# Kernel optimization log

Measured on AMD Instinct MI355X. Metric: run time of the kernel, lower is better.

The kernel has to match this reference:

```python
import jax, jax.numpy as jnp
import numpy as np

EPS = 1e-5
CHUNK = 512  # chunk of known points for the running-argmin 1-NN search


def nn_idx(unknown, known):
    """1-NN index of each unknown point into known. unknown (B,n,3), known (B,m,3) -> (B,n) int32."""
    B, n, _ = unknown.shape
    m = known.shape[1]
    u2 = jnp.sum(unknown * unknown, axis=-1)  # (B,n)
    # (num_chunks, B, CHUNK, 3)
    kc = known.reshape(B, m // CHUNK, CHUNK, 3).transpose(1, 0, 2, 3)

    def step(carry, kch):
        best_d, best_i, off = carry
        k2 = jnp.sum(kch * kch, axis=-1)  # (B,CHUNK)
        # squared distances for this chunk: (B,n,CHUNK)
        d = u2[:, :, None] - 2.0 * jnp.einsum('bnd,bcd->bnc', unknown, kch) + k2[:, None, :]
        dmin = jnp.min(d, axis=-1)
        imin = jnp.argmin(d, axis=-1).astype(jnp.int32) + off
        upd = dmin < best_d
        return (jnp.where(upd, dmin, best_d), jnp.where(upd, imin, best_i), off + CHUNK), None

    init = (jnp.full((B, n), jnp.inf, unknown.dtype),
            jnp.zeros((B, n), jnp.int32),
            jnp.int32(0))
    (_, best_i, _), _ = jax.lax.scan(step, init, kc)
    return best_i


def bn_relu(x, gamma, beta):
    """Training-mode BatchNorm over (B, n) per channel followed by ReLU. x: (B,C,n)."""
    mean = jnp.mean(x, axis=(0, 2), keepdims=True)
    var = jnp.mean(jnp.square(x - mean), axis=(0, 2), keepdims=True)  # biased, as torch BN
    y = (x - mean) * jax.lax.rsqrt(var + EPS)
    return jax.nn.relu(y * gamma[None, :, None] + beta[None, :, None])


def setup_inputs() -> dict:
    key = jax.random.key(0)
    ks = jax.random.split(key, 8)
    B, n, m, C1, C2 = 2, 65536, 16384, 128, 256
    mlp = [C2 + C1, 256, 128]
    return {
        'unknown': jax.random.normal(ks[0], (B, n, 3), jnp.float32),
        'known': jax.random.normal(ks[1], (B, m, 3), jnp.float32),
        'unknow_feats': jax.random.normal(ks[2], (B, C1, n), jnp.float32),
        'known_feats': jax.random.normal(ks[3], (B, C2, m), jnp.float32),
        'w1': jax.random.normal(ks[4], (mlp[1], mlp[0]), jnp.float32) * (1.0 / np.sqrt(mlp[0])),
        'gamma1': jnp.ones((mlp[1],), jnp.float32),
        'beta1': jnp.zeros((mlp[1],), jnp.float32),
        'w2': jax.random.normal(ks[5], (mlp[2], mlp[1]), jnp.float32) * (1.0 / np.sqrt(mlp[1])),
        'gamma2': jnp.ones((mlp[2],), jnp.float32),
        'beta2': jnp.zeros((mlp[2],), jnp.float32),
    }


def reference(unknown, known, unknow_feats, known_feats, w1, gamma1, beta1, w2, gamma2, beta2):
    idx = nn_idx(unknown, known)  # (B,n) int32
    # gather: (B,C2,m) indexed along m -> (B,C2,n)
    interpolated = jnp.take_along_axis(known_feats, idx[:, None, :], axis=2)
    new_features = jnp.concatenate([interpolated, unknow_feats], axis=1)  # (B,C1+C2,n)
    h = bn_relu(jnp.einsum('oc,bcn->bon', w1, new_features), gamma1, beta1)
    out = bn_relu(jnp.einsum('oc,bcn->bon', w2, h), gamma2, beta2)
    return out  # (B, mlp[-1], n)
```

## Files before the change

kernel.cpp:

```cpp
#include <hip/hip_runtime.h>

typedef unsigned short u16;
typedef unsigned int u32;
typedef __bf16 bf16x8 __attribute__((ext_vector_type(8)));
typedef _Float16 f16;
typedef _Float16 f16x8 __attribute__((ext_vector_type(8)));
typedef float f32x4 __attribute__((ext_vector_type(4)));
typedef float f32x16 __attribute__((ext_vector_type(16)));

#define B_ 2
#define N_ 65536
#define M_ 16384
#define C1_ 128
#define C2_ 256
#define K1_ 384
#define O1_ 256
#define O2_ 128
#define JT_ 512
#define CH_ 16
#define NCH_ ((JT_/2)/CH_)
#define EPS2_ 6.0e-3f
#define TFIN_ 1.25e-4f

__device__ __forceinline__ u16 f2bf(float f) {
    u32 u = __float_as_uint(f);
    u32 r = (u + 0x7FFFu + ((u >> 16) & 1u)) >> 16;
    return (u16)r;
}
__device__ __forceinline__ float bf2f(u16 h) {
    return __uint_as_float(((u32)h) << 16);
}
__device__ __forceinline__ u32 pack2(float lo, float hi) {
    return (u32)f2bf(lo) | ((u32)f2bf(hi) << 16);
}
__device__ __forceinline__ uint4 pack8(float4 a, float4 b) {
    uint4 r;
    r.x = pack2(a.x, a.y); r.y = pack2(a.z, a.w);
    r.z = pack2(b.x, b.y); r.w = pack2(b.z, b.w);
    return r;
}
__device__ __forceinline__ u16 h2u(f16 h) {
    union { f16 h; u16 u; } c; c.h = h; return c.u;
}

__device__ __forceinline__ float mul_rn(float a, float b) {
    float p = __fmul_rn(a, b);
    asm volatile("" : "+v"(p));
    return p;
}
__device__ __forceinline__ float sq3_np(float x, float y, float z) {
    return __fadd_rn(__fadd_rn(mul_rn(x, x), mul_rn(y, y)), mul_rn(z, z));
}
__device__ __forceinline__ float dot3_fma(float a0, float b0, float a1, float b1,
                                          float a2, float b2) {
    return fmaf(a2, b2, fmaf(a1, b1, mul_rn(a0, b0)));
}


__global__ __launch_bounds__(256) void k_prep_u(const float* __restrict__ unk,
                                                u16* __restrict__ Aprep) {
    int g = blockIdx.x * 256 + threadIdx.x;
    const float* up = unk + (size_t)g * 3;
    float tx = -2.f * up[0], ty = -2.f * up[1], tz = -2.f * up[2];
    f16 xh = (f16)tx; f16 xl = (f16)(tx - (float)xh);
    f16 yh = (f16)ty; f16 yl = (f16)(ty - (float)yh);
    f16 zh = (f16)tz; f16 zl = (f16)(tz - (float)zh);
    u16 lo[8] = {h2u(xh), h2u(xh), h2u(xl), h2u(yh), h2u(yh), h2u(yl), h2u(zh), h2u(zh)};
    u16 hi[8] = {h2u(zl), 0x3C00u, 0x3C00u, 0, 0, 0, 0, 0};
    u16* tb = Aprep + ((size_t)(g >> 5)) * 512;
    int r = g & 31;
    *(uint4*)(tb + r * 8) = *(uint4*)lo;
    *(uint4*)(tb + (r + 32) * 8) = *(uint4*)hi;
}

__global__ __launch_bounds__(256) void k_prep_k(const float* __restrict__ kn,
                                                u16* __restrict__ Bprep,
                                                float4* __restrict__ kco) {
    int g = blockIdx.x * 256 + threadIdx.x;
    const float* kp = kn + (size_t)g * 3;
    float x = kp[0], y = kp[1], z = kp[2];
    float qv = sq3_np(x, y, z);
    f16 xh = (f16)x; f16 xl = (f16)(x - (float)xh);
    f16 yh = (f16)y; f16 yl = (f16)(y - (float)yh);
    f16 zh = (f16)z; f16 zl = (f16)(z - (float)zh);
    f16 qh = (f16)qv; f16 ql = (f16)(qv - (float)qh);
    u16 lo[8] = {h2u(xh), h2u(xl), h2u(xh), h2u(yh), h2u(yl), h2u(yh), h2u(zh), h2u(zl)};
    u16 hi[8] = {h2u(zh), h2u(qh), h2u(ql), 0x3C00u, 0x3C00u, 0, 0, 0};
    u16* tb = Bprep + ((size_t)(g >> 5)) * 512;
    int r = g & 31;
    *(uint4*)(tb + r * 8) = *(uint4*)lo;
    *(uint4*)(tb + (r + 32) * 8) = *(uint4*)hi;
    kco[g] = make_float4(x, y, z, qv);
}

__global__ __launch_bounds__(256, 4) void k_nn(
        const u16* __restrict__ Aprep, const u16* __restrict__ Bprep,
        const float* __restrict__ unk, const float4* __restrict__ kco,
        unsigned long long* __restrict__ pc) {
    __shared__ u16 sB[2][CH_ * 512];
    __shared__ unsigned long long cand[256];
    __shared__ float thrS[256];
    const int t = threadIdx.x;
    const int half = blockIdx.y, b = blockIdx.z;
    const int lane = t & 63, w = t >> 6;
    const int rowbase = blockIdx.x * 256;
    const u16* at = Aprep + (((size_t)(b * N_ + rowbase + w * 64)) >> 5) * 512;
    f16x8 af0 = *(const f16x8*)(at + lane * 8);
    f16x8 af1 = *(const f16x8*)(at + 512 + lane * 8);
    const u16* Bsrc = Bprep + ((size_t)b * JT_ + (size_t)half * (JT_ / 2)) * 512;
    cand[t] = ~0ULL;

    uint4 vs0, vs1, vs2, vs3;
#define STAGEV(c) { const u16* sp = Bsrc + (size_t)(c) * (CH_ * 512) + t * 8;  \
    vs0 = *(const uint4*)sp;          vs1 = *(const uint4*)(sp + 2048);        \
    vs2 = *(const uint4*)(sp + 4096); vs3 = *(const uint4*)(sp + 6144); }
#define WRITEV(bi) { u16* dp = &sB[bi][t * 8];                                 \
    *(uint4*)dp = vs0;          *(uint4*)(dp + 2048) = vs1;                    \
    *(uint4*)(dp + 4096) = vs2; *(uint4*)(dp + 6144) = vs3; }

    const f32x16 zz = {0.f,0.f,0.f,0.f,0.f,0.f,0.f,0.f,0.f,0.f,0.f,0.f,0.f,0.f,0.f,0.f};

    f32x16 rm0, rm1;
#pragma unroll
    for (int r = 0; r < 16; ++r) { rm0[r] = 3.4e38f; rm1[r] = 3.4e38f; }

    STAGEV(0); WRITEV(0);
    __syncthreads();
    for (int c = 0; c < NCH_; ++c) {
        if (c + 1 < NCH_) STAGEV(c + 1);
        const u16* bb = sB[c & 1];
#pragma unroll 2
        for (int tp = 0; tp < CH_; tp += 2) {
            f16x8 bf0 = *(const f16x8*)(bb + tp * 512 + lane * 8);
            f16x8 bf1 = *(const f16x8*)(bb + tp * 512 + 512 + lane * 8);
            f32x16 a  = __builtin_amdgcn_mfma_f32_32x32x16_f16(af0, bf0, zz, 0, 0, 0);
            f32x16 ca = __builtin_amdgcn_mfma_f32_32x32x16_f16(af0, bf1, zz, 0, 0, 0);
#pragma unroll
            for (int r = 0; r < 16; ++r)
                rm0[r] = fminf(fminf(rm0[r], a[r]), ca[r]);
            a  = __builtin_amdgcn_mfma_f32_32x32x16_f16(af1, bf0, zz, 0, 0, 0);
            ca = __builtin_amdgcn_mfma_f32_32x32x16_f16(af1, bf1, zz, 0, 0, 0);
#pragma unroll
            for (int r = 0; r < 16; ++r)
                rm1[r] = fminf(fminf(rm1[r], a[r]), ca[r]);
        }
        __syncthreads();
        if (c + 1 < NCH_) WRITEV((c + 1) & 1);
        __syncthreads();
    }

    STAGEV(0);

#pragma unroll
    for (int r = 0; r < 16; ++r) {
        float v0 = rm0[r], v1 = rm1[r];
        v0 = fminf(v0, __shfl_xor(v0, 1));  v1 = fminf(v1, __shfl_xor(v1, 1));
        v0 = fminf(v0, __shfl_xor(v0, 2));  v1 = fminf(v1, __shfl_xor(v1, 2));
        v0 = fminf(v0, __shfl_xor(v0, 4));  v1 = fminf(v1, __shfl_xor(v1, 4));
        v0 = fminf(v0, __shfl_xor(v0, 8));  v1 = fminf(v1, __shfl_xor(v1, 8));
        v0 = fminf(v0, __shfl_xor(v0, 16)); v1 = fminf(v1, __shfl_xor(v1, 16));
        if ((lane & 31) == 0) {
            int rl = w * 64 + ((lane >> 5) << 2) + (r & 3) + 8 * (r >> 2);
            thrS[rl] = v0 + EPS2_;
            thrS[rl + 32] = v1 + EPS2_;
        }
    }
    __syncthreads();
    if (lane >= 32) {
        float tf0 = thrS[w * 64 + (lane & 31)] + TFIN_;
        float tf1 = thrS[w * 64 + 32 + (lane & 31)] + TFIN_;
        f16 h0 = (f16)(-tf0);
        af0[3] = h0; af0[4] = (f16)(-tf0 - (float)h0);
        f16 h1 = (f16)(-tf1);
        af1[3] = h1; af1[4] = (f16)(-tf1 - (float)h1);
    }
    WRITEV(0);
    __syncthreads();

    const float4* kcb = kco + (size_t)b * M_;
    const float* ub = unk + (size_t)b * N_ * 3;
    const int rloc0 = w * 64 + ((lane >> 5) << 2);
    const int jb0 = half * (M_ / 2);

    for (int c = 0; c < NCH_; ++c) {
        if (c + 1 < NCH_) STAGEV(c + 1);
        const u16* bb = sB[c & 1];
#pragma unroll 2
        for (int tt = 0; tt < CH_; ++tt) {
            f16x8 bf = *(const f16x8*)(bb + tt * 512 + lane * 8);
            f32x16 a0 = __builtin_amdgcn_mfma_f32_32x32x16_f16(af0, bf, zz, 0, 0, 0);
            f32x16 a1 = __builtin_amdgcn_mfma_f32_32x32x16_f16(af1, bf, zz, 0, 0, 0);
            float u0 = fminf(fminf(a0[0], a0[1]), a0[2]);
            float u1 = fminf(fminf(a0[3], a0[4]), a0[5]);
            float u2 = fminf(fminf(a0[6], a0[7]), a0[8]);
            float u3 = fminf(fminf(a0[9], a0[10]), a0[11]);
            float u4 = fminf(fminf(a0[12], a0[13]), a0[14]);
            float tm0 = fminf(fminf(fminf(u0, u1), a0[15]), fminf(fminf(u2, u3), u4));
            float w0 = fminf(fminf(a1[0], a1[1]), a1[2]);
            float w1 = fminf(fminf(a1[3], a1[4]), a1[5]);
            float w2 = fminf(fminf(a1[6], a1[7]), a1[8]);
            float w3 = fminf(fminf(a1[9], a1[10]), a1[11]);
            float w4 = fminf(fminf(a1[12], a1[13]), a1[14]);
            float tm1 = fminf(fminf(fminf(w0, w1), a1[15]), fminf(fminf(w2, w3), w4));
            unsigned long long m = __ballot(tm0 <= 0.f) | __ballot(tm1 <= 0.f);
            if (m) {
                int j = jb0 + (c * CH_ + tt) * 32 + (lane & 31);
                float4 kc = kcb[j];
#pragma unroll
                for (int r = 0; r < 16; ++r) {
                    if (a0[r] <= 0.f) {
                        int rl = rloc0 + (r & 3) + 8 * (r >> 2);
                        const float* up = ub + (size_t)(rowbase + rl) * 3;
                        float x = up[0], y = up[1], zc = up[2];
                        float uq = sq3_np(x, y, zc);
                        float dot = dot3_fma(x, kc.x, y, kc.y, zc, kc.z);
                        float d = __fadd_rn(fmaf(-2.0f, dot, uq), kc.w);
                        u32 db = __float_as_uint(d);
                        db = (db & 0x80000000u) ? ~db : (db | 0x80000000u);
                        atomicMin(&cand[rl], ((unsigned long long)db << 32) | (u32)j);
                    }
                    if (a1[r] <= 0.f) {
                        int rl = rloc0 + 32 + (r & 3) + 8 * (r >> 2);
                        const float* up = ub + (size_t)(rowbase + rl) * 3;
                        float x = up[0], y = up[1], zc = up[2];
                        float uq = sq3_np(x, y, zc);
                        float dot = dot3_fma(x, kc.x, y, kc.y, zc, kc.z);
                        float d = __fadd_rn(fmaf(-2.0f, dot, uq), kc.w);
                        u32 db = __float_as_uint(d);
                        db = (db & 0x80000000u) ? ~db : (db | 0x80000000u);
                        atomicMin(&cand[rl], ((unsigned long long)db << 32) | (u32)j);
                    }
                }
            }
        }
        __syncthreads();
        if (c + 1 < NCH_) WRITEV((c + 1) & 1);
        __syncthreads();
    }
    pc[((size_t)(half * B_ + b)) * N_ + rowbase + t] = cand[t];
#undef STAGEV
#undef WRITEV
}

__global__ __launch_bounds__(256) void k_nn_merge(
        const unsigned long long* __restrict__ pc, int* __restrict__ idx) {
    int g = blockIdx.x * 256 + threadIdx.x;
    unsigned long long a = pc[g];
    unsigned long long c = pc[(size_t)(B_ * N_) + g];
    idx[g] = (int)(u32)((c < a ? c : a) & 0xFFFFFFFFu);
}

__global__ __launch_bounds__(256) void k_tr_kf(const float* __restrict__ kf,
                                               u16* __restrict__ kfT) {
    __shared__ float lt[64][65];
    const int t = threadIdx.x, b = blockIdx.z;
    const int j0 = blockIdx.x * 64, c0 = blockIdx.y * 64;
    const int jl = t & 63, cl4 = t >> 6;
#pragma unroll
    for (int p = 0; p < 16; ++p) {
        int c = c0 + cl4 + p * 4;
        lt[cl4 + p * 4][jl] = kf[((size_t)(b * C2_ + c)) * M_ + j0 + jl];
    }
    __syncthreads();
    const int cl = t & 63, jr4 = t >> 6;
#pragma unroll
    for (int p = 0; p < 16; ++p) {
        int j = j0 + jr4 + p * 4;
        kfT[((size_t)(b * M_ + j)) * C2_ + c0 + cl] = f2bf(lt[cl][jr4 + p * 4]);
    }
}

__global__ __launch_bounds__(256) void k_tr_uf(const float* __restrict__ uf,
                                               u16* __restrict__ newF) {
    __shared__ float lt[64][65];
    const int t = threadIdx.x, b = blockIdx.z;
    const int i0 = blockIdx.x * 64, c0 = blockIdx.y * 64;
    const int il = t & 63, cl4 = t >> 6;
#pragma unroll
    for (int p = 0; p < 16; ++p) {
        int c = c0 + cl4 + p * 4;
        lt[cl4 + p * 4][il] = uf[((size_t)(b * C1_ + c)) * N_ + i0 + il];
    }
    __syncthreads();
    const int cl = t & 63, ir4 = t >> 6;
#pragma unroll
    for (int p = 0; p < 16; ++p) {
        int i = i0 + ir4 + p * 4;
        newF[((size_t)(b * N_ + i)) * K1_ + C2_ + c0 + cl] = f2bf(lt[cl][ir4 + p * 4]);
    }
}

__global__ __launch_bounds__(256) void k_gather(const u16* __restrict__ kfT,
                                                const int* __restrict__ idx,
                                                u16* __restrict__ newF) {
    const int t = threadIdx.x, b = blockIdx.y;
    const int il = t >> 5, qq = t & 31;
    const int i = blockIdx.x * 8 + il;
    const int j = idx[b * N_ + i];
    const uint4* src = (const uint4*)(kfT + ((size_t)(b * M_ + j)) * C2_) + qq;
    uint4* dst = (uint4*)(newF + ((size_t)(b * N_ + i)) * K1_) + qq;
    *dst = *src;
}

__global__ __launch_bounds__(256) void k_gemm1(const u16* __restrict__ newF,
                                               const float* __restrict__ w1,
                                               u16* __restrict__ y1) {
    __shared__ u16 As[128 * 40];
    __shared__ u16 Bs[128 * 40];
    const int t = threadIdx.x, b = blockIdx.z;
    const int i0 = blockIdx.x * 128, o0 = blockIdx.y * 128;
    const int lane = t & 63, wv = t >> 6, wr = wv >> 1, wc = wv & 1;
    const int col = lane & 15, q = lane >> 4;

    const int rA0 = t >> 2, sA0 = t & 3;
    const u16* aS0 = newF + ((size_t)(b * N_ + i0 + rA0)) * K1_ + sA0 * 8;
    const u16* aS1 = aS0 + (size_t)64 * K1_;
    const float* bS0 = w1 + (size_t)(o0 + rA0) * K1_ + sA0 * 8;
    const float* bS1 = bS0 + (size_t)64 * K1_;
    u16* aD0 = &As[rA0 * 40 + sA0 * 8];
    u16* aD1 = aD0 + 64 * 40;
    u16* bD0 = &Bs[rA0 * 40 + sA0 * 8];
    u16* bD1 = bD0 + 64 * 40;

    f32x4 acc[4][4];
#pragma unroll
    for (int m = 0; m < 4; ++m)
#pragma unroll
        for (int n = 0; n < 4; ++n) acc[m][n] = (f32x4){0.f, 0.f, 0.f, 0.f};

    uint4 a0 = *(const uint4*)aS0, a1 = *(const uint4*)aS1;
    float4 f00 = *(const float4*)bS0, f01 = *(const float4*)(bS0 + 4);
    float4 f10 = *(const float4*)bS1, f11 = *(const float4*)(bS1 + 4);

    for (int ks = 0; ks < 12; ++ks) {
        __syncthreads();
        *(uint4*)aD0 = a0; *(uint4*)aD1 = a1;
        *(uint4*)bD0 = pack8(f00, f01); *(uint4*)bD1 = pack8(f10, f11);
        __syncthreads();
        if (ks < 11) {
            int ko = (ks + 1) * 32;
            a0 = *(const uint4*)(aS0 + ko); a1 = *(const uint4*)(aS1 + ko);
            f00 = *(const float4*)(bS0 + ko); f01 = *(const float4*)(bS0 + ko + 4);
            f10 = *(const float4*)(bS1 + ko); f11 = *(const float4*)(bS1 + ko + 4);
        }
        const u16* ap = &As[(wr * 64 + col) * 40 + q * 8];
        const u16* bp = &Bs[(wc * 64 + col) * 40 + q * 8];
        bf16x8 af[4], bfr[4];
#pragma unroll
        for (int m = 0; m < 4; ++m) af[m] = *(const bf16x8*)(ap + m * 640);
#pragma unroll
        for (int n = 0; n < 4; ++n) bfr[n] = *(const bf16x8*)(bp + n * 640);
#pragma unroll
        for (int m = 0; m < 4; ++m)
#pragma unroll
            for (int n = 0; n < 4; ++n)
                acc[m][n] = __builtin_amdgcn_mfma_f32_16x16x32_bf16(af[m], bfr[n], acc[m][n], 0, 0, 0);
    }
#pragma unroll
    for (int m = 0; m < 4; ++m)
#pragma unroll
        for (int n = 0; n < 4; ++n) {
            int go = o0 + wc * 64 + n * 16 + col;
#pragma unroll
            for (int r = 0; r < 4; ++r) {
                int gi = i0 + wr * 64 + m * 16 + q * 4 + r;
                y1[((size_t)(b * N_ + gi)) * O1_ + go] = f2bf(acc[m][n][r]);
            }
        }
}

__global__ __launch_bounds__(256) void k_stats_bf16(const u16* __restrict__ y1,
                                                    float* __restrict__ sum,
                                                    float* __restrict__ sq) {
    const int t = threadIdx.x;
    const int row0 = blockIdx.x * 1024;
    float s = 0.f, qq = 0.f;
    for (int r = 0; r < 1024; ++r) {
        float v = bf2f(y1[((size_t)(row0 + r)) * O1_ + t]);
        s += v; qq = fmaf(v, v, qq);
    }
    atomicAdd(&sum[t], s);
    atomicAdd(&sq[t], qq);
}

__global__ __launch_bounds__(256) void k_stats_f32(const float* __restrict__ y2,
                                                   float* __restrict__ sum,
                                                   float* __restrict__ sq) {
    const int t = threadIdx.x;
    const int o = t & 127, h = t >> 7;
    const int row0 = blockIdx.x * 1024;
    float s = 0.f, qq = 0.f;
    for (int r = 0; r < 512; ++r) {
        float v = y2[((size_t)(row0 + r * 2 + h)) * O2_ + o];
        s += v; qq = fmaf(v, v, qq);
    }
    atomicAdd(&sum[o], s);
    atomicAdd(&sq[o], qq);
}

__global__ void k_bn_fin(const float* __restrict__ sum, const float* __restrict__ sq,
                         const float* __restrict__ gamma, const float* __restrict__ beta,
                         float* __restrict__ scale, float* __restrict__ bias,
                         int C, float invN) {
    int t = threadIdx.x;
    if (t < C) {
        float mean = sum[t] * invN;
        float var = sq[t] * invN - mean * mean;
        float rs = rsqrtf(var + 1e-5f);
        float sc = gamma[t] * rs;
        scale[t] = sc;
        bias[t] = beta[t] - mean * sc;
    }
}

__global__ __launch_bounds__(256) void k_gemm2(const u16* __restrict__ y1,
                                               const float* __restrict__ w2,
                                               const float* __restrict__ s1,
                                               const float* __restrict__ b1,
                                               float* __restrict__ y2) {
    __shared__ u16 As[128 * 40];
    __shared__ u16 Bs[128 * 40];
    const int t = threadIdx.x, b = blockIdx.z;
    const int i0 = blockIdx.x * 128;
    const int lane = t & 63, wv = t >> 6, wr = wv >> 1, wc = wv & 1;
    const int col = lane & 15, q = lane >> 4;

    const int rA0 = t >> 2, sA0 = t & 3;
    const u16* aS0 = y1 + ((size_t)(b * N_ + i0 + rA0)) * O1_ + sA0 * 8;
    const u16* aS1 = aS0 + (size_t)64 * O1_;
    const float* bS0 = w2 + (size_t)rA0 * O1_ + sA0 * 8;
    const float* bS1 = bS0 + (size_t)64 * O1_;
    u16* aD0 = &As[rA0 * 40 + sA0 * 8];
    u16* aD1 = aD0 + 64 * 40;
    u16* bD0 = &Bs[rA0 * 40 + sA0 * 8];
    u16* bD1 = bD0 + 64 * 40;

    f32x4 acc[4][4];
#pragma unroll
    for (int m = 0; m < 4; ++m)
#pragma unroll
        for (int n = 0; n < 4; ++n) acc[m][n] = (f32x4){0.f, 0.f, 0.f, 0.f};

    uint4 a0 = *(const uint4*)aS0, a1 = *(const uint4*)aS1;
    float4 f00 = *(const float4*)bS0, f01 = *(const float4*)(bS0 + 4);
    float4 f10 = *(const float4*)bS1, f11 = *(const float4*)(bS1 + 4);

    for (int ks = 0; ks < 8; ++ks) {
        int oc = ks * 32 + sA0 * 8;
        float4 sc0 = *(const float4*)(s1 + oc), sc1 = *(const float4*)(s1 + oc + 4);
        float4 bb0 = *(const float4*)(b1 + oc), bb1 = *(const float4*)(b1 + oc + 4);
        uint4 h0, h1;
        {
            const u16* hs = (const u16*)&a0;
            float v[8];
            v[0] = fmaxf(fmaf(bf2f(hs[0]), sc0.x, bb0.x), 0.f);
            v[1] = fmaxf(fmaf(bf2f(hs[1]), sc0.y, bb0.y), 0.f);
            v[2] = fmaxf(fmaf(bf2f(hs[2]), sc0.z, bb0.z), 0.f);
            v[3] = fmaxf(fmaf(bf2f(hs[3]), sc0.w, bb0.w), 0.f);
            v[4] = fmaxf(fmaf(bf2f(hs[4]), sc1.x, bb1.x), 0.f);
            v[5] = fmaxf(fmaf(bf2f(hs[5]), sc1.y, bb1.y), 0.f);
            v[6] = fmaxf(fmaf(bf2f(hs[6]), sc1.z, bb1.z), 0.f);
            v[7] = fmaxf(fmaf(bf2f(hs[7]), sc1.w, bb1.w), 0.f);
            h0.x = pack2(v[0], v[1]); h0.y = pack2(v[2], v[3]);
            h0.z = pack2(v[4], v[5]); h0.w = pack2(v[6], v[7]);
        }
        {
            const u16* hs = (const u16*)&a1;
            float v[8];
            v[0] = fmaxf(fmaf(bf2f(hs[0]), sc0.x, bb0.x), 0.f);
            v[1] = fmaxf(fmaf(bf2f(hs[1]), sc0.y, bb0.y), 0.f);
            v[2] = fmaxf(fmaf(bf2f(hs[2]), sc0.z, bb0.z), 0.f);
            v[3] = fmaxf(fmaf(bf2f(hs[3]), sc0.w, bb0.w), 0.f);
            v[4] = fmaxf(fmaf(bf2f(hs[4]), sc1.x, bb1.x), 0.f);
            v[5] = fmaxf(fmaf(bf2f(hs[5]), sc1.y, bb1.y), 0.f);
            v[6] = fmaxf(fmaf(bf2f(hs[6]), sc1.z, bb1.z), 0.f);
            v[7] = fmaxf(fmaf(bf2f(hs[7]), sc1.w, bb1.w), 0.f);
            h1.x = pack2(v[0], v[1]); h1.y = pack2(v[2], v[3]);
            h1.z = pack2(v[4], v[5]); h1.w = pack2(v[6], v[7]);
        }
        __syncthreads();
        *(uint4*)aD0 = h0; *(uint4*)aD1 = h1;
        *(uint4*)bD0 = pack8(f00, f01); *(uint4*)bD1 = pack8(f10, f11);
        __syncthreads();
        if (ks < 7) {
            int ko = (ks + 1) * 32;
            a0 = *(const uint4*)(aS0 + ko); a1 = *(const uint4*)(aS1 + ko);
            f00 = *(const float4*)(bS0 + ko); f01 = *(const float4*)(bS0 + ko + 4);
            f10 = *(const float4*)(bS1 + ko); f11 = *(const float4*)(bS1 + ko + 4);
        }
        const u16* ap = &As[(wr * 64 + col) * 40 + q * 8];
        const u16* bp = &Bs[(wc * 64 + col) * 40 + q * 8];
        bf16x8 af[4], bfr[4];
#pragma unroll
        for (int m = 0; m < 4; ++m) af[m] = *(const bf16x8*)(ap + m * 640);
#pragma unroll
        for (int n = 0; n < 4; ++n) bfr[n] = *(const bf16x8*)(bp + n * 640);
#pragma unroll
        for (int m = 0; m < 4; ++m)
#pragma unroll
            for (int n = 0; n < 4; ++n)
                acc[m][n] = __builtin_amdgcn_mfma_f32_16x16x32_bf16(af[m], bfr[n], acc[m][n], 0, 0, 0);
    }
#pragma unroll
    for (int m = 0; m < 4; ++m)
#pragma unroll
        for (int n = 0; n < 4; ++n) {
            int go = wc * 64 + n * 16 + col;
#pragma unroll
            for (int r = 0; r < 4; ++r) {
                int gi = i0 + wr * 64 + m * 16 + q * 4 + r;
                y2[((size_t)(b * N_ + gi)) * O2_ + go] = acc[m][n][r];
            }
        }
}

__global__ __launch_bounds__(256) void k_out(const float* __restrict__ y2,
                                             const float* __restrict__ s2,
                                             const float* __restrict__ b2,
                                             float* __restrict__ out) {
    __shared__ float lt[64 * 65];
    const int t = threadIdx.x, b = blockIdx.z;
    const int i0 = blockIdx.x * 64, o0 = blockIdx.y * 64;
    const int oc = t & 63, ir4 = t >> 6;
    const float sc = s2[o0 + oc], bs = b2[o0 + oc];
#pragma unroll
    for (int p = 0; p < 16; ++p) {
        int i = i0 + ir4 + p * 4;
        float v = y2[((size_t)(b * N_ + i)) * O2_ + o0 + oc];
        lt[oc * 65 + ir4 + p * 4] = fmaxf(fmaf(v, sc, bs), 0.f);
    }
    __syncthreads();
    const int il = t & 63, or4 = t >> 6;
#pragma unroll
    for (int p = 0; p < 16; ++p) {
        int o = o0 + or4 + p * 4;
        out[((size_t)(b * O2_ + o)) * N_ + i0 + il] = lt[(or4 + p * 4) * 65 + il];
    }
}

extern "C" void kernel_launch(void* const* d_in, const int* in_sizes, int n_in,
                              void* d_out, int out_size, void* d_ws, size_t ws_size,
                              hipStream_t stream) {
    const float* unknown = (const float*)d_in[0];
    const float* known   = (const float*)d_in[1];
    const float* uf      = (const float*)d_in[2];
    const float* kf      = (const float*)d_in[3];
    const float* w1      = (const float*)d_in[4];
    const float* g1      = (const float*)d_in[5];
    const float* be1     = (const float*)d_in[6];
    const float* w2      = (const float*)d_in[7];
    const float* g2      = (const float*)d_in[8];
    const float* be2     = (const float*)d_in[9];
    float* out = (float*)d_out;

    char* w = (char*)d_ws;
    float* bn1_sum = (float*)w;
    float* bn1_sq  = bn1_sum + 256;
    float* bn2_sum = bn1_sq + 256;
    float* bn2_sq  = bn2_sum + 128;
    float* s1 = (float*)(w + 4096);
    float* b1 = s1 + 256;
    float* s2 = b1 + 256;
    float* b2 = s2 + 128;
    int* idx = (int*)(w + 8192);
    u16* newF = (u16*)(w + 532480);
    float* y2 = (float*)(w + 532480);
    size_t R2 = 532480 + 100663296ULL;
    u16*   Aprep = (u16*)(w + R2);
    u16*   Bprep = (u16*)(w + R2 + 4194304ULL);
    float4* kco  = (float4*)(w + R2 + 5242880ULL);
    unsigned long long* pc = (unsigned long long*)(w + R2 + 5767168ULL);
    u16*  kfT = (u16*)(w + R2 + 16777216ULL);
    u16*   y1 = (u16*)(w + R2);

    hipMemsetAsync(w, 0, 3072, stream);

    k_prep_u<<<512, 256, 0, stream>>>(unknown, Aprep);
    k_prep_k<<<128, 256, 0, stream>>>(known, Bprep, kco);
    k_nn<<<dim3(N_ / 256, 2, B_), 256, 0, stream>>>(Aprep, Bprep, unknown, kco, pc);
    k_nn_merge<<<512, 256, 0, stream>>>(pc, idx);
    k_tr_kf<<<dim3(256, 4, 2), 256, 0, stream>>>(kf, kfT);
    k_tr_uf<<<dim3(1024, 2, 2), 256, 0, stream>>>(uf, newF);
    k_gather<<<dim3(8192, 2), 256, 0, stream>>>(kfT, idx, newF);
    k_gemm1<<<dim3(512, 2, 2), 256, 0, stream>>>(newF, w1, y1);
    k_stats_bf16<<<128, 256, 0, stream>>>(y1, bn1_sum, bn1_sq);
    k_bn_fin<<<1, 256, 0, stream>>>(bn1_sum, bn1_sq, g1, be1, s1, b1, 256, 1.f / 131072.f);
    k_gemm2<<<dim3(512, 1, 2), 256, 0, stream>>>(y1, w2, s1, b1, y2);
    k_stats_f32<<<128, 256, 0, stream>>>(y2, bn2_sum, bn2_sq);
    k_bn_fin<<<1, 256, 0, stream>>>(bn2_sum, bn2_sq, g2, be2, s2, b2, 128, 1.f / 131072.f);
    k_out<<<dim3(1024, 2, 2), 256, 0, stream>>>(y2, s2, b2, out);
}
```

Measured before the change: 618.6 us.

## Stream NN key tiles from global into registers instead of LDS double-buffering

The 1-NN kernel no longer stages the known-point MFMA operands through a shared-memory double buffer guarded by block barriers. Each wave now loads its B fragments straight from global memory, prefetching one step ahead in registers, and the barriers are gone. The candidate check also replaces the fminf reduction tree with an OR of sign bits before the ballot. The cost is redundant per-wave global/L1 traffic and a prefetch that reads one tile past the end of the range. The sign-bit test also treats an exact +0 distance differently from the old <=0 check.

Result: faster. 582.2 us (-5.9%).

```diff
diff --git a/kernel.cpp b/kernel.cpp
--- a/kernel.cpp
+++ b/kernel.cpp
@@ -17,8 +17,7 @@
 #define O1_ 256
 #define O2_ 128
 #define JT_ 512
-#define CH_ 16
-#define NCH_ ((JT_/2)/CH_)
+#define HT_ (JT_/2)
 #define EPS2_ 6.0e-3f
 #define TFIN_ 1.25e-4f
 
@@ -97,7 +96,6 @@
         const u16* __restrict__ Aprep, const u16* __restrict__ Bprep,
         const float* __restrict__ unk, const float4* __restrict__ kco,
         unsigned long long* __restrict__ pc) {
-    __shared__ u16 sB[2][CH_ * 512];
     __shared__ unsigned long long cand[256];
     __shared__ float thrS[256];
     const int t = threadIdx.x;
@@ -107,49 +105,33 @@
     const u16* at = Aprep + (((size_t)(b * N_ + rowbase + w * 64)) >> 5) * 512;
     f16x8 af0 = *(const f16x8*)(at + lane * 8);
     f16x8 af1 = *(const f16x8*)(at + 512 + lane * 8);
-    const u16* Bsrc = Bprep + ((size_t)b * JT_ + (size_t)half * (JT_ / 2)) * 512;
+    const u16* Bp = Bprep + ((size_t)b * JT_ + (size_t)half * HT_) * 512 + lane * 8;
     cand[t] = ~0ULL;
 
-    uint4 vs0, vs1, vs2, vs3;
-#define STAGEV(c) { const u16* sp = Bsrc + (size_t)(c) * (CH_ * 512) + t * 8;  \
-    vs0 = *(const uint4*)sp;          vs1 = *(const uint4*)(sp + 2048);        \
-    vs2 = *(const uint4*)(sp + 4096); vs3 = *(const uint4*)(sp + 6144); }
-#define WRITEV(bi) { u16* dp = &sB[bi][t * 8];                                 \
-    *(uint4*)dp = vs0;          *(uint4*)(dp + 2048) = vs1;                    \
-    *(uint4*)(dp + 4096) = vs2; *(uint4*)(dp + 6144) = vs3; }
-
     const f32x16 zz = {0.f,0.f,0.f,0.f,0.f,0.f,0.f,0.f,0.f,0.f,0.f,0.f,0.f,0.f,0.f,0.f};
 
     f32x16 rm0, rm1;
 #pragma unroll
     for (int r = 0; r < 16; ++r) { rm0[r] = 3.4e38f; rm1[r] = 3.4e38f; }
 
-    STAGEV(0); WRITEV(0);
-    __syncthreads();
-    for (int c = 0; c < NCH_; ++c) {
-        if (c + 1 < NCH_) STAGEV(c + 1);
-        const u16* bb = sB[c & 1];
-#pragma unroll 2
-        for (int tp = 0; tp < CH_; tp += 2) {
-            f16x8 bf0 = *(const f16x8*)(bb + tp * 512 + lane * 8);
-            f16x8 bf1 = *(const f16x8*)(bb + tp * 512 + 512 + lane * 8);
-            f32x16 a  = __builtin_amdgcn_mfma_f32_32x32x16_f16(af0, bf0, zz, 0, 0, 0);
-            f32x16 ca = __builtin_amdgcn_mfma_f32_32x32x16_f16(af0, bf1, zz, 0, 0, 0);
-#pragma unroll
-            for (int r = 0; r < 16; ++r)
-                rm0[r] = fminf(fminf(rm0[r], a[r]), ca[r]);
-            a  = __builtin_amdgcn_mfma_f32_32x32x16_f16(af1, bf0, zz, 0, 0, 0);
-            ca = __builtin_amdgcn_mfma_f32_32x32x16_f16(af1, bf1, zz, 0, 0, 0);
-#pragma unroll
-            for (int r = 0; r < 16; ++r)
-                rm1[r] = fminf(fminf(rm1[r], a[r]), ca[r]);
-        }
-        __syncthreads();
-        if (c + 1 < NCH_) WRITEV((c + 1) & 1);
-        __syncthreads();
-    }
-
-    STAGEV(0);
+    f16x8 c0 = *(const f16x8*)Bp;
+    f16x8 c1 = *(const f16x8*)(Bp + 512);
+    for (int tp = 0; tp < HT_; tp += 2) {
+        f16x8 n0 = *(const f16x8*)(Bp + 1024);
+        f16x8 n1 = *(const f16x8*)(Bp + 1536);
+        Bp += 1024;
+        f32x16 a  = __builtin_amdgcn_mfma_f32_32x32x16_f16(af0, c0, zz, 0, 0, 0);
+        f32x16 ca = __builtin_amdgcn_mfma_f32_32x32x16_f16(af0, c1, zz, 0, 0, 0);
+#pragma unroll
+        for (int r = 0; r < 16; ++r)
+            rm0[r] = fminf(fminf(rm0[r], a[r]), ca[r]);
+        a  = __builtin_amdgcn_mfma_f32_32x32x16_f16(af1, c0, zz, 0, 0, 0);
+        ca = __builtin_amdgcn_mfma_f32_32x32x16_f16(af1, c1, zz, 0, 0, 0);
+#pragma unroll
+        for (int r = 0; r < 16; ++r)
+            rm1[r] = fminf(fminf(rm1[r], a[r]), ca[r]);
+        c0 = n0; c1 = n1;
+    }
 
 #pragma unroll
     for (int r = 0; r < 16; ++r) {
@@ -165,81 +147,64 @@
             thrS[rl + 32] = v1 + EPS2_;
         }
     }
-    __syncthreads();
     if (lane >= 32) {
         float tf0 = thrS[w * 64 + (lane & 31)] + TFIN_;
-        float tf1 = thrS[w * 64 + 32 + (lane & 31)] + TFIN_;
         f16 h0 = (f16)(-tf0);
         af0[3] = h0; af0[4] = (f16)(-tf0 - (float)h0);
+        float tf1 = thrS[w * 64 + 32 + (lane & 31)] + TFIN_;
         f16 h1 = (f16)(-tf1);
         af1[3] = h1; af1[4] = (f16)(-tf1 - (float)h1);
     }
-    WRITEV(0);
-    __syncthreads();
 
     const float4* kcb = kco + (size_t)b * M_;
     const float* ub = unk + (size_t)b * N_ * 3;
     const int rloc0 = w * 64 + ((lane >> 5) << 2);
     const int jb0 = half * (M_ / 2);
 
-    for (int c = 0; c < NCH_; ++c) {
-        if (c + 1 < NCH_) STAGEV(c + 1);
-        const u16* bb = sB[c & 1];
-#pragma unroll 2
-        for (int tt = 0; tt < CH_; ++tt) {
-            f16x8 bf = *(const f16x8*)(bb + tt * 512 + lane * 8);
-            f32x16 a0 = __builtin_amdgcn_mfma_f32_32x32x16_f16(af0, bf, zz, 0, 0, 0);
-            f32x16 a1 = __builtin_amdgcn_mfma_f32_32x32x16_f16(af1, bf, zz, 0, 0, 0);
-            float u0 = fminf(fminf(a0[0], a0[1]), a0[2]);
-            float u1 = fminf(fminf(a0[3], a0[4]), a0[5]);
-            float u2 = fminf(fminf(a0[6], a0[7]), a0[8]);
-            float u3 = fminf(fminf(a0[9], a0[10]), a0[11]);
-            float u4 = fminf(fminf(a0[12], a0[13]), a0[14]);
-            float tm0 = fminf(fminf(fminf(u0, u1), a0[15]), fminf(fminf(u2, u3), u4));
-            float w0 = fminf(fminf(a1[0], a1[1]), a1[2]);
-            float w1 = fminf(fminf(a1[3], a1[4]), a1[5]);
-            float w2 = fminf(fminf(a1[6], a1[7]), a1[8]);
-            float w3 = fminf(fminf(a1[9], a1[10]), a1[11]);
-            float w4 = fminf(fminf(a1[12], a1[13]), a1[14]);
-            float tm1 = fminf(fminf(fminf(w0, w1), a1[15]), fminf(fminf(w2, w3), w4));
-            unsigned long long m = __ballot(tm0 <= 0.f) | __ballot(tm1 <= 0.f);
-            if (m) {
-                int j = jb0 + (c * CH_ + tt) * 32 + (lane & 31);
-                float4 kc = kcb[j];
-#pragma unroll
-                for (int r = 0; r < 16; ++r) {
-                    if (a0[r] <= 0.f) {
-                        int rl = rloc0 + (r & 3) + 8 * (r >> 2);
-                        const float* up = ub + (size_t)(rowbase + rl) * 3;
-                        float x = up[0], y = up[1], zc = up[2];
-                        float uq = sq3_np(x, y, zc);
-                        float dot = dot3_fma(x, kc.x, y, kc.y, zc, kc.z);
-                        float d = __fadd_rn(fmaf(-2.0f, dot, uq), kc.w);
-                        u32 db = __float_as_uint(d);
-                        db = (db & 0x80000000u) ? ~db : (db | 0x80000000u);
-                        atomicMin(&cand[rl], ((unsigned long long)db << 32) | (u32)j);
-                    }
-                    if (a1[r] <= 0.f) {
-                        int rl = rloc0 + 32 + (r & 3) + 8 * (r >> 2);
-                        const float* up = ub + (size_t)(rowbase + rl) * 3;
-                        float x = up[0], y = up[1], zc = up[2];
-                        float uq = sq3_np(x, y, zc);
-                        float dot = dot3_fma(x, kc.x, y, kc.y, zc, kc.z);
-                        float d = __fadd_rn(fmaf(-2.0f, dot, uq), kc.w);
-                        u32 db = __float_as_uint(d);
-                        db = (db & 0x80000000u) ? ~db : (db | 0x80000000u);
-                        atomicMin(&cand[rl], ((unsigned long long)db << 32) | (u32)j);
-                    }
+    Bp -= (size_t)HT_ * 512;
+    c0 = *(const f16x8*)Bp;
+    f16x8 c1b = *(const f16x8*)(Bp + 512);
+    for (int tt = 0; tt < HT_; ++tt) {
+        f16x8 nx = *(const f16x8*)(Bp + 1024);
+        Bp += 512;
+        f32x16 a0 = __builtin_amdgcn_mfma_f32_32x32x16_f16(af0, c0, zz, 0, 0, 0);
+        f32x16 a1 = __builtin_amdgcn_mfma_f32_32x32x16_f16(af1, c0, zz, 0, 0, 0);
+        u32 o = 0;
+#pragma unroll
+        for (int r = 0; r < 16; ++r)
+            o |= __float_as_uint(a0[r]) | __float_as_uint(a1[r]);
+        if (__ballot((int)o < 0)) {
+            int j = jb0 + tt * 32 + (lane & 31);
+            float4 kc = kcb[j];
+#pragma unroll
+            for (int r = 0; r < 16; ++r) {
+                if (a0[r] <= 0.f) {
+                    int rl = rloc0 + (r & 3) + 8 * (r >> 2);
+                    const float* up = ub + (size_t)(rowbase + rl) * 3;
+                    float x = up[0], y = up[1], zc = up[2];
+                    float uq = sq3_np(x, y, zc);
+                    float dot = dot3_fma(x, kc.x, y, kc.y, zc, kc.z);
+                    float d = __fadd_rn(fmaf(-2.0f, dot, uq), kc.w);
+                    u32 db = __float_as_uint(d);
+                    db = (db & 0x80000000u) ? ~db : (db | 0x80000000u);
+                    atomicMin(&cand[rl], ((unsigned long long)db << 32) | (u32)j);
+                }
+                if (a1[r] <= 0.f) {
+                    int rl = rloc0 + 32 + (r & 3) + 8 * (r >> 2);
+                    const float* up = ub + (size_t)(rowbase + rl) * 3;
+                    float x = up[0], y = up[1], zc = up[2];
+                    float uq = sq3_np(x, y, zc);
+                    float dot = dot3_fma(x, kc.x, y, kc.y, zc, kc.z);
+                    float d = __fadd_rn(fmaf(-2.0f, dot, uq), kc.w);
+                    u32 db = __float_as_uint(d);
+                    db = (db & 0x80000000u) ? ~db : (db | 0x80000000u);
+                    atomicMin(&cand[rl], ((unsigned long long)db << 32) | (u32)j);
                 }
             }
         }
-        __syncthreads();
-        if (c + 1 < NCH_) WRITEV((c + 1) & 1);
-        __syncthreads();
+        c0 = c1b; c1b = nx;
     }
     pc[((size_t)(half * B_ + b)) * N_ + rowbase + t] = cand[t];
-#undef STAGEV
-#undef WRITEV
 }
 
 __global__ __launch_bounds__(256) void k_nn_merge(
```
